# Optimization experiments

Hardware: AMD Instinct MI355X
Metric: run time of the kernel (lower is better)

Reference implementation:

```python
import jax, jax.numpy as jnp
import numpy as np
from jax import lax

NPIX = 256        # charge grid size
OS = 3            # oversample / stride
KS = 9            # dynamic kernel window size (3 * OS)
TIME_STEPS = 8
ORDER = 2

# polynomial powers: all (px, py) with px + py <= ORDER, shape (2, n_terms)
_pairs = [(i, s - i) for s in range(ORDER + 1) for i in range(s + 1)]
POWERS = jnp.asarray(np.array(_pairs).T, dtype=jnp.float32)  # (2, 6)
NTERMS = POWERS.shape[1]
NFEAT = 2 * NTERMS  # 12 encoder output channels


def pixel_coords(n, diameter):
    # dLux-style pixel center coordinates, shape (2, n, n)
    pitch = diameter / n
    c = ((jnp.arange(n) - (n - 1) / 2.0) * pitch).astype(jnp.float32)
    return jnp.stack(jnp.meshgrid(c, c, indexing="ij"))


def downsample(x, n, mean):
    h, w = x.shape
    r = x.reshape(h // n, n, w // n, n)
    return r.mean((1, 3)) if mean else r.sum((1, 3))


def conv2d_same(x, w):
    # x: (C, H, W), w: (O, C, 3, 3), SAME padding, no bias
    return lax.conv_general_dilated(
        x[None], w, (1, 1), "SAME",
        dimension_numbers=("NCHW", "OIHW", "NCHW"))[0]


def calc_kernels(coords):
    # coords: (npix, npix, 2, 3, 3) distorted sub-pixel centers
    npix = coords.shape[0]
    # full[c, 3i+p, 3j+q] = coords[i, j, c, p, q]  (kernels_to_array over both channels)
    full = coords.transpose(2, 0, 3, 1, 4).reshape(2, OS * npix, OS * npix)
    pc31 = pixel_coords(3, 1.0)                      # (2, 3, 3)
    empty = jnp.tile(pc31, (1, npix + 2, npix + 2))  # (2, 3(npix+2), 3(npix+2))
    padded = empty.at[:, 3:-3, 3:-3].set(full)
    rel = jnp.repeat(jnp.repeat(pixel_coords(3, 3.0), 3, axis=1), 3, axis=2)  # (2, 9, 9)
    win = jnp.stack([
        jnp.stack([padded[:, u:u + 3 * npix - 2:3, v:v + 3 * npix - 2:3]
                   for v in range(KS)], axis=1)
        for u in range(KS)], axis=1)                 # (2, 9, 9, npix, npix)
    x = win[0] + rel[0][..., None, None]
    y = win[1] + rel[1][..., None, None]
    size = jnp.float32(1.0 / 3.0)
    # overlap of a size x size box at (x, y) with the unit box centered at 0
    ox = jnp.maximum(0.0, jnp.minimum(x + size / 2, 0.5) - jnp.maximum(x - size / 2, -0.5))
    oy = jnp.maximum(0.0, jnp.minimum(y + size / 2, 0.5) - jnp.maximum(y - size / 2, -0.5))
    frac = ox * oy / (size * size)                   # (9, 9, npix, npix)
    return frac.transpose(2, 3, 0, 1)                # (npix, npix, 9, 9)


def dfn_kernels(charge, w1, w2, w3):
    # encoder: conv(1->32) relu conv(32->32) relu conv(32->12)
    f = jax.nn.relu(conv2d_same(charge[None], w1))
    f = jax.nn.relu(conv2d_same(f, w2))
    f = conv2d_same(f, w3)                           # (12, npix, npix)
    npix = charge.shape[-1]
    coeffs = f.reshape(2, NTERMS, npix, npix)        # per-pixel (2, n_terms)
    knots = pixel_coords(3, 1.0)                     # (2, 3, 3)
    pow_base = (knots[0][None] ** POWERS[0][:, None, None]) * \
               (knots[1][None] ** POWERS[1][:, None, None])   # (n_terms, 3, 3)
    distortion = jnp.einsum("ctij,txy->ijcxy", coeffs, pow_base)
    coords = knots[None, None] + distortion          # (npix, npix, 2, 3, 3)
    return calc_kernels(coords)


def apply_kernels_stride(illum, kernels):
    # illum: (3*npix, 3*npix); kernels: (npix, npix, 9, 9)
    npix = kernels.shape[0]
    pad = KS // OS  # 3
    ip = jnp.pad(illum, pad)
    out = jnp.zeros((npix, npix), illum.dtype)
    for u in range(KS):          # fixed 9x9 offset loop, each iter fully vectorized
        for v in range(KS):
            out = out + ip[u:u + 3 * npix - 2:3, v:v + 3 * npix - 2:3] * kernels[:, :, u, v]
    return out


def setup_inputs() -> dict:
    key = jax.random.key(0)
    ks = jax.random.split(key, 6)
    return {
        "bias": jax.random.normal(ks[0], (NPIX, NPIX), jnp.float32),
        "illuminance": jax.random.uniform(ks[1], (3 * NPIX, 3 * NPIX), jnp.float32),
        "sensitivity": jax.random.uniform(ks[2], (3 * NPIX, 3 * NPIX), jnp.float32),
        "w1": 0.05 * jax.random.normal(ks[3], (32, 1, 3, 3), jnp.float32),
        "w2": 0.05 * jax.random.normal(ks[4], (32, 32, 3, 3), jnp.float32),
        "w3": 0.05 * jax.random.normal(ks[5], (NFEAT, 32, 3, 3), jnp.float32),
    }


def reference(bias, illuminance, sensitivity, w1, w2, w3):
    illum_full = illuminance / TIME_STEPS
    illum = downsample(sensitivity * illum_full, OS, mean=False)   # (npix, npix)
    sens = downsample(sensitivity, OS, mean=True)                  # (npix, npix)
    charge = bias - jnp.mean(bias)                                 # use_bias=True
    charges = [charge]
    diffusions = []
    for _ in range(TIME_STEPS):  # bleed=True path
        norm_charge = charge - jnp.mean(charge)
        kernels = dfn_kernels(norm_charge, w1, w2, w3)
        new_charge = sens * apply_kernels_stride(illum_full, kernels)
        charge = charge + new_charge
        diffusions.append(illum - new_charge)
        charges.append(charge)
    ramp = jnp.stack(charges) + jnp.median(bias)                   # (T+1, npix, npix)
    return ramp, jnp.stack(diffusions)                             # (T, npix, npix)
```

## Files before the change

### kernel.cpp

```cpp
#include <hip/hip_runtime.h>

#define N2 65536
#define FW 768

#define WS_CHARGE 0
#define WS_ILLUM  (N2)
#define WS_SENS   (2*N2)
#define WS_FEAT2  (3*N2)
#define WS_W1T    (35*N2)
#define WS_W2T    (WS_W1T + 288)
#define WS_W3T    (WS_W2T + 9216)
#define WS_SUMS   (WS_W3T + 3456)
#define WS_BSUM   (WS_SUMS + 9)
#define WS_MEANB  (WS_SUMS + 10)
#define WS_MEDIAN (WS_SUMS + 11)
#define WS_SEL    (WS_SUMS + 12)
#define WS_H1     (WS_SUMS + 16)
#define WS_H2     (WS_H1 + 4096)
#define WS_H3     (WS_H2 + 2048)
#define NCLEAR    (16 + 4096 + 2048 + 2048)

__device__ __forceinline__ void block_sum_atomic(float v, float* dst){
  #pragma unroll
  for (int o = 32; o > 0; o >>= 1) v += __shfl_down(v, o, 64);
  __shared__ float red[16];
  int lane = threadIdx.x & 63, wid = threadIdx.x >> 6;
  int nw = (int)(blockDim.x >> 6);
  if (lane == 0) red[wid] = v;
  __syncthreads();
  if (threadIdx.x == 0){
    float s = red[0];
    for (int w = 1; w < nw; w++) s += red[w];
    atomicAdd(dst, s);
  }
}

__device__ __forceinline__ unsigned block_scan_u32(unsigned v, unsigned* wsum){
  __syncthreads();
  int lane = threadIdx.x & 63, wid = threadIdx.x >> 6, nw = (int)(blockDim.x >> 6);
  unsigned x = v;
  #pragma unroll
  for (int o = 1; o < 64; o <<= 1){ unsigned y = __shfl_up(x, o, 64); if (lane >= o) x += y; }
  if (lane == 63) wsum[wid] = x;
  __syncthreads();
  if (wid == 0){
    unsigned w = (lane < nw) ? wsum[lane] : 0u;
    #pragma unroll
    for (int o = 1; o < 16; o <<= 1){ unsigned y = __shfl_up(w, o, 64); if (lane >= o) w += y; }
    if (lane < nw) wsum[lane] = w;
  }
  __syncthreads();
  unsigned base = (wid > 0) ? wsum[wid - 1] : 0u;
  return base + x;
}

__device__ __forceinline__ unsigned key_flip(unsigned u){
  return (u & 0x80000000u) ? ~u : (u ^ 0x80000000u);
}

__global__ __launch_bounds__(256) void k_prep(const float* __restrict__ w1,
    const float* __restrict__ w2, const float* __restrict__ w3,
    float* __restrict__ ws){
  int t = blockIdx.x * 256 + threadIdx.x;
  unsigned* z = (unsigned*)(ws + WS_SUMS);
  for (int i = t; i < NCLEAR; i += 2048) z[i] = 0u;
  for (int idx = t; idx < 288; idx += 2048){
    int co = idx / 9, k = idx - co*9;
    ws[WS_W1T + k*32 + co] = w1[idx];
  }
  for (int idx = t; idx < 9216; idx += 2048){
    int co = idx / 288, r = idx - co*288, ci = r / 9, k = r - ci*9;
    ws[WS_W2T + (ci*9 + k)*32 + co] = w2[idx];
  }
  for (int idx = t; idx < 3456; idx += 2048){
    int co = idx / 288, r = idx - co*288, ci = r / 9, k = r - ci*9;
    ws[WS_W3T + (ci*9 + k)*12 + co] = w3[idx];
  }
}

__global__ __launch_bounds__(256) void k_h1(const float* __restrict__ bias,
                                            float* __restrict__ ws){
  unsigned* H1 = (unsigned*)(ws + WS_H1);
  float s = 0.f;
  for (int i = blockIdx.x * 256 + threadIdx.x; i < N2; i += 64*256){
    float v = bias[i]; s += v;
    atomicAdd(&H1[key_flip(__float_as_uint(v)) >> 20], 1u);
  }
  block_sum_atomic(s, ws + WS_BSUM);
}

__global__ __launch_bounds__(1024) void k_s1(float* __restrict__ ws){
  const unsigned* H1 = (const unsigned*)(ws + WS_H1);
  unsigned* sel = (unsigned*)(ws + WS_SEL);
  __shared__ unsigned wssc[16];
  int t = threadIdx.x;
  uint4 h4 = ((const uint4*)H1)[t];
  unsigned c4 = h4.x + h4.y + h4.z + h4.w;
  unsigned cum = block_scan_u32(c4, wssc);
  unsigned before = cum - c4;
  unsigned hh[4] = {h4.x, h4.y, h4.z, h4.w};
  for (int s = 0; s < 2; s++){
    unsigned rank = 32767u + (unsigned)s;
    if (before <= rank && rank < cum){
      unsigned kk = rank - before, acc = 0; unsigned b = 0;
      for (; b < 3; b++){ if (acc + hh[b] > kk) break; acc += hh[b]; }
      sel[s]     = 4u*(unsigned)t + b;
      sel[2 + s] = kk - acc;
    }
  }
  if (t == 0) ws[WS_MEANB] = ws[WS_BSUM] * (1.f / (float)N2);
}

__global__ __launch_bounds__(256) void k_h23(const float* __restrict__ bias,
    float* __restrict__ ws, unsigned* __restrict__ H, int shift){
  const unsigned* sel = (const unsigned*)(ws + WS_SEL);
  unsigned p0 = sel[0], p1 = sel[1];
  for (int i = blockIdx.x * 256 + threadIdx.x; i < N2; i += 64*256){
    unsigned key = key_flip(__float_as_uint(bias[i]));
    unsigned top = key >> (shift + 10);
    unsigned bin = (key >> shift) & 1023u;
    if (top == p0) atomicAdd(&H[bin], 1u);
    if (top == p1) atomicAdd(&H[1024u + bin], 1u);
  }
}

__global__ __launch_bounds__(1024) void k_s23(float* __restrict__ ws,
    const unsigned* __restrict__ H, int final_lvl){
  unsigned* sel = (unsigned*)(ws + WS_SEL);
  __shared__ unsigned wssc[16];
  __shared__ float meds[2];
  int t = threadIdx.x;
  for (int s = 0; s < 2; s++){
    unsigned cc = H[s*1024 + t];
    unsigned rank = sel[2 + s];
    unsigned cum = block_scan_u32(cc, wssc);
    unsigned before = cum - cc;
    if (before <= rank && rank < cum){
      unsigned p = (sel[s] << 10) | (unsigned)t;
      sel[s]     = p;
      sel[2 + s] = rank - before;
      if (final_lvl){
        unsigned u = (p & 0x80000000u) ? (p ^ 0x80000000u) : ~p;
        meds[s] = __uint_as_float(u);
      }
    }
    __syncthreads();
  }
  if (final_lvl && t == 0) ws[WS_MEDIAN] = 0.5f * (meds[0] + meds[1]);
}

__global__ __launch_bounds__(256) void k_init(const float* __restrict__ bias,
    const float* __restrict__ illum, const float* __restrict__ sens,
    float* __restrict__ ws, float* __restrict__ out){
  int pix = blockIdx.x * 256 + threadIdx.x;
  int i = pix >> 8, j = pix & 255;
  float si = 0.f, ss = 0.f;
  #pragma unroll
  for (int p = 0; p < 3; p++)
    #pragma unroll
    for (int q = 0; q < 3; q++){
      float se = sens[(3*i+p)*FW + 3*j+q];
      float il = illum[(3*i+p)*FW + 3*j+q];
      si = fmaf(se, il * 0.125f, si);
      ss += se;
    }
  ws[WS_ILLUM + pix] = si;
  ws[WS_SENS  + pix] = ss * (1.f/9.f);
  float c = bias[pix] - ws[WS_MEANB];
  ws[WS_CHARGE + pix] = c;
  out[pix] = c + ws[WS_MEDIAN];
  block_sum_atomic(c, ws + WS_SUMS + 0);
}

__global__ __launch_bounds__(512) void k_convA(float* __restrict__ ws,
    const float* __restrict__ w1t, const float* __restrict__ w2t, int step){
  __shared__ float chg[400];
  __shared__ float f1[32*360];
  const float* charge = ws + WS_CHARGE;
  const float mean = ws[WS_SUMS + step] * (1.f / (float)N2);
  const int gi0 = (blockIdx.x >> 4) << 4, gj0 = (blockIdx.x & 15) << 4;
  const int tid = threadIdx.x;

  if (tid < 400){
    int r = tid / 20, c = tid - r*20;
    int gi = gi0 + r - 2, gj = gj0 + c - 2;
    float v = 0.f;
    if ((unsigned)gi < 256u && (unsigned)gj < 256u) v = charge[(gi<<8) + gj] - mean;
    chg[tid] = v;
  }
  __syncthreads();

  if (tid < 324){
    int r = tid / 18, c = tid - r*18;
    int gi = gi0 + r - 1, gj = gj0 + c - 1;
    float acc[32];
    #pragma unroll
    for (int co = 0; co < 32; co++) acc[co] = 0.f;
    if ((unsigned)gi < 256u && (unsigned)gj < 256u){
      float x[9];
      #pragma unroll
      for (int dy = 0; dy < 3; dy++)
        #pragma unroll
        for (int dx = 0; dx < 3; dx++) x[dy*3+dx] = chg[(r+dy)*20 + c+dx];
      #pragma unroll
      for (int k = 0; k < 9; k++){
        float xv = x[k];
        const float4* wr = (const float4*)(w1t + k*32);
        #pragma unroll
        for (int g = 0; g < 8; g++){
          float4 w4 = wr[g];
          acc[g*4+0] = fmaf(w4.x, xv, acc[g*4+0]);
          acc[g*4+1] = fmaf(w4.y, xv, acc[g*4+1]);
          acc[g*4+2] = fmaf(w4.z, xv, acc[g*4+2]);
          acc[g*4+3] = fmaf(w4.w, xv, acc[g*4+3]);
        }
      }
      #pragma unroll
      for (int co = 0; co < 32; co++) acc[co] = fmaxf(acc[co], 0.f);
    }
    #pragma unroll
    for (int co = 0; co < 32; co++) f1[co*360 + r*20 + c] = acc[co];
  }
  __syncthreads();

  const int lane = tid & 63;
  const int co4 = __builtin_amdgcn_readfirstlane((tid >> 6) << 2);
  const int ti = lane >> 2, tjc = (lane & 3) << 2;
  float acc[4][4];
  #pragma unroll
  for (int p = 0; p < 4; p++)
    #pragma unroll
    for (int cc = 0; cc < 4; cc++) acc[p][cc] = 0.f;

  const float* wb = w2t + co4;
  for (int ci = 0; ci < 32; ci++){
    float xr[3][6];
    #pragma unroll
    for (int dy = 0; dy < 3; dy++){
      const float* rp = f1 + ci*360 + (ti+dy)*20 + tjc;
      float4 a = *(const float4*)rp;
      float2 b = *(const float2*)(rp + 4);
      xr[dy][0] = a.x; xr[dy][1] = a.y; xr[dy][2] = a.z; xr[dy][3] = a.w;
      xr[dy][4] = b.x; xr[dy][5] = b.y;
    }
    const float* wci = wb + ci*288;
    #pragma unroll
    for (int k = 0; k < 9; k++){
      const int dy = k / 3, dx = k - dy*3;
      float4 w4 = *(const float4*)(wci + k*32);
      #pragma unroll
      for (int p = 0; p < 4; p++){
        float xv = xr[dy][p + dx];
        acc[p][0] = fmaf(w4.x, xv, acc[p][0]);
        acc[p][1] = fmaf(w4.y, xv, acc[p][1]);
        acc[p][2] = fmaf(w4.z, xv, acc[p][2]);
        acc[p][3] = fmaf(w4.w, xv, acc[p][3]);
      }
    }
  }
  float* f2 = ws + WS_FEAT2;
  const int prow = ((gi0 + ti) << 8) + gj0 + tjc;
  #pragma unroll
  for (int cc = 0; cc < 4; cc++){
    float4 v;
    v.x = fmaxf(acc[0][cc], 0.f);
    v.y = fmaxf(acc[1][cc], 0.f);
    v.z = fmaxf(acc[2][cc], 0.f);
    v.w = fmaxf(acc[3][cc], 0.f);
    *(float4*)(f2 + (co4 + cc)*N2 + prow) = v;
  }
}

__global__ __launch_bounds__(512) void k_convB(float* __restrict__ ws,
    const float* __restrict__ w3t, const float* __restrict__ illum,
    float* __restrict__ out, int step){
  __shared__ float tile[32*400];
  __shared__ float S[9*324];
  const float* f2 = ws + WS_FEAT2;
  const int gi0 = (blockIdx.x >> 4) << 4, gj0 = (blockIdx.x & 15) << 4;
  const int tid = threadIdx.x;

  for (int idx = tid; idx < 32*400; idx += 512){
    int ci = idx / 400, px = idx - ci*400, r = px / 20, c = px - r*20;
    int gi = gi0 + r - 2, gj = gj0 + c - 2;
    float v = 0.f;
    if ((unsigned)gi < 256u && (unsigned)gj < 256u) v = f2[ci*N2 + (gi<<8) + gj];
    tile[idx] = v;
  }
  __syncthreads();

  if (tid < 324){
    int a = tid / 18, b = tid - a*18;
    int gi = gi0 + a - 1, gj = gj0 + b - 1;
    float Sv[9];
    #pragma unroll
    for (int d = 0; d < 9; d++) Sv[d] = 0.f;
    if ((unsigned)gi < 256u && (unsigned)gj < 256u){
      float cf[12];
      #pragma unroll
      for (int co = 0; co < 12; co++) cf[co] = 0.f;
      for (int ci = 0; ci < 32; ci++){
        float x[9];
        #pragma unroll
        for (int dy = 0; dy < 3; dy++)
          #pragma unroll
          for (int dx = 0; dx < 3; dx++) x[dy*3+dx] = tile[ci*400 + (a+dy)*20 + (b+dx)];
        #pragma unroll
        for (int k = 0; k < 9; k++){
          const float4* wr = (const float4*)(w3t + (ci*9 + k)*12);
          float4 A = wr[0], B = wr[1], C = wr[2];
          float xv = x[k];
          cf[0] = fmaf(A.x, xv, cf[0]);   cf[1] = fmaf(A.y, xv, cf[1]);
          cf[2] = fmaf(A.z, xv, cf[2]);   cf[3] = fmaf(A.w, xv, cf[3]);
          cf[4] = fmaf(B.x, xv, cf[4]);   cf[5] = fmaf(B.y, xv, cf[5]);
          cf[6] = fmaf(B.z, xv, cf[6]);   cf[7] = fmaf(B.w, xv, cf[7]);
          cf[8] = fmaf(C.x, xv, cf[8]);   cf[9] = fmaf(C.y, xv, cf[9]);
          cf[10] = fmaf(C.z, xv, cf[10]); cf[11] = fmaf(C.w, xv, cf[11]);
        }
      }
      const float third = 1.f/3.f, sixth = 1.f/6.f;
      #pragma unroll
      for (int p = 0; p < 3; p++){
        float kx = (p - 1) * third;
        #pragma unroll
        for (int q = 0; q < 3; q++){
          float ky = (q - 1) * third;
          float cx = kx + cf[0] + cf[1]*ky + cf[2]*kx + cf[3]*ky*ky + cf[4]*kx*ky + cf[5]*kx*kx;
          float cy = ky + cf[6] + cf[7]*ky + cf[8]*kx + cf[9]*ky*ky + cf[10]*kx*ky + cf[11]*kx*kx;
          float Ipq = illum[(3*gi+p)*FW + 3*gj+q] * 0.125f;
          float ox[3], oy[3];
          #pragma unroll
          for (int d = 0; d < 3; d++){
            float xx = cx + (float)(d - 1);
            ox[d] = fmaxf(0.f, fminf(xx + sixth, 0.5f) - fmaxf(xx - sixth, -0.5f));
            float yy = cy + (float)(d - 1);
            oy[d] = fmaxf(0.f, fminf(yy + sixth, 0.5f) - fmaxf(yy - sixth, -0.5f));
          }
          #pragma unroll
          for (int d = 0; d < 3; d++){
            float aa = Ipq * ox[d];
            #pragma unroll
            for (int e = 0; e < 3; e++) Sv[d*3+e] = fmaf(aa, oy[e], Sv[d*3+e]);
          }
        }
      }
    }
    #pragma unroll
    for (int d = 0; d < 9; d++) S[d*324 + tid] = Sv[d];
  }
  __syncthreads();

  float chv = 0.f;
  if (tid < 256){
    int ti = tid >> 4, tj = tid & 15;
    float s = 0.f;
    #pragma unroll
    for (int d = 0; d < 3; d++)
      #pragma unroll
      for (int e = 0; e < 3; e++) s += S[(d*3+e)*324 + (ti+d)*18 + tj+e];
    int pix = ((gi0 + ti) << 8) + gj0 + tj;
    float nc = ws[WS_SENS + pix] * (9.f * s);
    float ch = ws[WS_CHARGE + pix] + nc;
    ws[WS_CHARGE + pix] = ch;
    out[(step + 1)*N2 + pix] = ch + ws[WS_MEDIAN];
    out[(9 + step)*N2 + pix] = ws[WS_ILLUM + pix] - nc;
    chv = ch;
  }
  block_sum_atomic(chv, ws + WS_SUMS + step + 1);
}

extern "C" void kernel_launch(void* const* d_in, const int* in_sizes, int n_in,
                              void* d_out, int out_size, void* d_ws, size_t ws_size,
                              hipStream_t stream) {
  (void)in_sizes; (void)n_in; (void)out_size; (void)ws_size;
  const float* bias  = (const float*)d_in[0];
  const float* illum = (const float*)d_in[1];
  const float* sens  = (const float*)d_in[2];
  const float* w1    = (const float*)d_in[3];
  const float* w2    = (const float*)d_in[4];
  const float* w3    = (const float*)d_in[5];
  float* out = (float*)d_out;
  float* ws  = (float*)d_ws;
  unsigned* H2 = (unsigned*)(ws + WS_H2);
  unsigned* H3 = (unsigned*)(ws + WS_H3);

  k_prep<<<8,   256, 0, stream>>>(w1, w2, w3, ws);
  k_h1  <<<64,  256, 0, stream>>>(bias, ws);
  k_s1  <<<1,  1024, 0, stream>>>(ws);
  k_h23 <<<64,  256, 0, stream>>>(bias, ws, H2, 10);
  k_s23 <<<1,  1024, 0, stream>>>(ws, H2, 0);
  k_h23 <<<64,  256, 0, stream>>>(bias, ws, H3, 0);
  k_s23 <<<1,  1024, 0, stream>>>(ws, H3, 1);
  k_init<<<256, 256, 0, stream>>>(bias, illum, sens, ws, out);
  for (int t = 0; t < 8; t++){
    k_convA<<<256, 512, 0, stream>>>(ws, ws + WS_W1T, ws + WS_W2T, t);
    k_convB<<<256, 512, 0, stream>>>(ws, ws + WS_W3T, illum, out, t);
  }
}
```

Baseline: 648.6 us.

## Split convA output channels across two blocks and privatize median histogram

```diff
diff --git a/kernel.cpp b/kernel.cpp
--- a/kernel.cpp
+++ b/kernel.cpp
@@ -15,10 +15,10 @@
 #define WS_MEANB  (WS_SUMS + 10)
 #define WS_MEDIAN (WS_SUMS + 11)
 #define WS_SEL    (WS_SUMS + 12)
-#define WS_H1     (WS_SUMS + 16)
-#define WS_H2     (WS_H1 + 4096)
+#define WS_H2     (WS_SUMS + 16)
 #define WS_H3     (WS_H2 + 2048)
-#define NCLEAR    (16 + 4096 + 2048 + 2048)
+#define NCLEAR    (16 + 2048 + 2048)
+#define WS_H1     (WS_H3 + 2048)
 
 __device__ __forceinline__ void block_sum_atomic(float v, float* dst){
   #pragma unroll
@@ -80,12 +80,17 @@
 
 __global__ __launch_bounds__(256) void k_h1(const float* __restrict__ bias,
                                             float* __restrict__ ws){
-  unsigned* H1 = (unsigned*)(ws + WS_H1);
+  __shared__ unsigned h[4096];
+  for (int i = threadIdx.x; i < 4096; i += 256) h[i] = 0u;
+  __syncthreads();
   float s = 0.f;
-  for (int i = blockIdx.x * 256 + threadIdx.x; i < N2; i += 64*256){
+  for (int i = blockIdx.x * 256 + threadIdx.x; i < N2; i += 32*256){
     float v = bias[i]; s += v;
-    atomicAdd(&H1[key_flip(__float_as_uint(v)) >> 20], 1u);
-  }
+    atomicAdd(&h[key_flip(__float_as_uint(v)) >> 20], 1u);
+  }
+  __syncthreads();
+  unsigned* H1 = (unsigned*)(ws + WS_H1) + (blockIdx.x << 12);
+  for (int i = threadIdx.x; i < 4096; i += 256) H1[i] = h[i];
   block_sum_atomic(s, ws + WS_BSUM);
 }
 
@@ -94,11 +99,15 @@
   unsigned* sel = (unsigned*)(ws + WS_SEL);
   __shared__ unsigned wssc[16];
   int t = threadIdx.x;
-  uint4 h4 = ((const uint4*)H1)[t];
-  unsigned c4 = h4.x + h4.y + h4.z + h4.w;
+  uint4 hv = make_uint4(0u, 0u, 0u, 0u);
+  for (int b = 0; b < 32; b++){
+    uint4 v = ((const uint4*)(H1 + (b << 12)))[t];
+    hv.x += v.x; hv.y += v.y; hv.z += v.z; hv.w += v.w;
+  }
+  unsigned c4 = hv.x + hv.y + hv.z + hv.w;
   unsigned cum = block_scan_u32(c4, wssc);
   unsigned before = cum - c4;
-  unsigned hh[4] = {h4.x, h4.y, h4.z, h4.w};
+  unsigned hh[4] = {hv.x, hv.y, hv.z, hv.w};
   for (int s = 0; s < 2; s++){
     unsigned rank = 32767u + (unsigned)s;
     if (before <= rank && rank < cum){
@@ -178,7 +187,9 @@
   __shared__ float f1[32*360];
   const float* charge = ws + WS_CHARGE;
   const float mean = ws[WS_SUMS + step] * (1.f / (float)N2);
-  const int gi0 = (blockIdx.x >> 4) << 4, gj0 = (blockIdx.x & 15) << 4;
+  const int tile = blockIdx.x >> 1;
+  const int half = blockIdx.x & 1;
+  const int gi0 = (tile >> 4) << 4, gj0 = (tile & 15) << 4;
   const int tid = threadIdx.x;
 
   if (tid < 400){
@@ -224,15 +235,13 @@
   __syncthreads();
 
   const int lane = tid & 63;
-  const int co4 = __builtin_amdgcn_readfirstlane((tid >> 6) << 2);
+  const int co2 = __builtin_amdgcn_readfirstlane(half*16 + ((tid >> 6) << 1));
   const int ti = lane >> 2, tjc = (lane & 3) << 2;
-  float acc[4][4];
+  float acc[4][2];
   #pragma unroll
-  for (int p = 0; p < 4; p++)
-    #pragma unroll
-    for (int cc = 0; cc < 4; cc++) acc[p][cc] = 0.f;
-
-  const float* wb = w2t + co4;
+  for (int p = 0; p < 4; p++){ acc[p][0] = 0.f; acc[p][1] = 0.f; }
+
+  const float* wb = w2t + co2;
   for (int ci = 0; ci < 32; ci++){
     float xr[3][6];
     #pragma unroll
@@ -247,27 +256,25 @@
     #pragma unroll
     for (int k = 0; k < 9; k++){
       const int dy = k / 3, dx = k - dy*3;
-      float4 w4 = *(const float4*)(wci + k*32);
+      float2 w2v = *(const float2*)(wci + k*32);
       #pragma unroll
       for (int p = 0; p < 4; p++){
         float xv = xr[dy][p + dx];
-        acc[p][0] = fmaf(w4.x, xv, acc[p][0]);
-        acc[p][1] = fmaf(w4.y, xv, acc[p][1]);
-        acc[p][2] = fmaf(w4.z, xv, acc[p][2]);
-        acc[p][3] = fmaf(w4.w, xv, acc[p][3]);
+        acc[p][0] = fmaf(w2v.x, xv, acc[p][0]);
+        acc[p][1] = fmaf(w2v.y, xv, acc[p][1]);
       }
     }
   }
   float* f2 = ws + WS_FEAT2;
   const int prow = ((gi0 + ti) << 8) + gj0 + tjc;
   #pragma unroll
-  for (int cc = 0; cc < 4; cc++){
+  for (int cc = 0; cc < 2; cc++){
     float4 v;
     v.x = fmaxf(acc[0][cc], 0.f);
     v.y = fmaxf(acc[1][cc], 0.f);
     v.z = fmaxf(acc[2][cc], 0.f);
     v.w = fmaxf(acc[3][cc], 0.f);
-    *(float4*)(f2 + (co4 + cc)*N2 + prow) = v;
+    *(float4*)(f2 + (co2 + cc)*N2 + prow) = v;
   }
 }
 
@@ -385,7 +392,7 @@
   unsigned* H3 = (unsigned*)(ws + WS_H3);
 
   k_prep<<<8,   256, 0, stream>>>(w1, w2, w3, ws);
-  k_h1  <<<64,  256, 0, stream>>>(bias, ws);
+  k_h1  <<<32,  256, 0, stream>>>(bias, ws);
   k_s1  <<<1,  1024, 0, stream>>>(ws);
   k_h23 <<<64,  256, 0, stream>>>(bias, ws, H2, 10);
   k_s23 <<<1,  1024, 0, stream>>>(ws, H2, 0);
@@ -393,7 +400,7 @@
   k_s23 <<<1,  1024, 0, stream>>>(ws, H3, 1);
   k_init<<<256, 256, 0, stream>>>(bias, illum, sens, ws, out);
   for (int t = 0; t < 8; t++){
-    k_convA<<<256, 512, 0, stream>>>(ws, ws + WS_W1T, ws + WS_W2T, t);
+    k_convA<<<512, 512, 0, stream>>>(ws, ws + WS_W1T, ws + WS_W2T, t);
     k_convB<<<256, 512, 0, stream>>>(ws, ws + WS_W3T, illum, out, t);
   }
 }
```

Measured after the change: 583.3 us. 10.1% less time.
